# Kernel tuning notes

Measured on AMD Instinct MI355X. Metric: run time of the kernel, lower is better.

Reference implementation:

```python
import jax, jax.numpy as jnp
import numpy as np

SIGMA = 1.0
KSIZE = 5
WEAK = 75.0
STRONG = 255.0
LOW_T = 0.00392
HIGH_T = 0.15

# scipy.signal.gaussian(M, std): unnormalized gaussian window
_n = np.arange(KSIZE, dtype=np.float32) - (KSIZE - 1) / 2.0
_g = np.exp(-0.5 * (_n / SIGMA) ** 2).astype(np.float32)
GAUSS_H = jnp.asarray(_g.reshape(1, 1, 1, KSIZE))  # horizontal 1xK
GAUSS_V = jnp.asarray(_g.reshape(1, 1, KSIZE, 1))  # vertical Kx1

_sobel = np.array([[1, 0, -1], [2, 0, -2], [1, 0, -1]], dtype=np.float32)
SOBEL_H = jnp.asarray(_sobel.reshape(1, 1, 3, 3))
SOBEL_V = jnp.asarray(_sobel.T.reshape(1, 1, 3, 3))

_f0 = np.array([[0, 0, 0], [0, 1, -1], [0, 0, 0]], np.float32)
_f45 = np.array([[0, 0, 0], [0, 1, 0], [0, 0, -1]], np.float32)
_f90 = np.array([[0, 0, 0], [0, 1, 0], [0, -1, 0]], np.float32)
_f135 = np.array([[0, 0, 0], [0, 1, 0], [-1, 0, 0]], np.float32)
_f180 = np.array([[0, 0, 0], [-1, 1, 0], [0, 0, 0]], np.float32)
_f225 = np.array([[-1, 0, 0], [0, 1, 0], [0, 0, 0]], np.float32)
_f270 = np.array([[0, -1, 0], [0, 1, 0], [0, 0, 0]], np.float32)
_f315 = np.array([[0, 0, -1], [0, 1, 0], [0, 0, 0]], np.float32)
DIR_FILT = jnp.asarray(np.stack([_f0, _f45, _f90, _f135, _f180, _f225, _f270, _f315]).reshape(8, 1, 3, 3))

NBR_FILT = jnp.asarray(np.array([[1, 1, 1], [1, 0, 1], [1, 1, 1]], np.float32).reshape(1, 1, 3, 3))


def _conv(x, w, pad):
    # cross-correlation, matching torch F.conv2d
    return jax.lax.conv_general_dilated(
        x, w, window_strides=(1, 1), padding=[(pad[0], pad[0]), (pad[1], pad[1])],
        dimension_numbers=('NCHW', 'OIHW', 'NCHW'))


def setup_inputs() -> dict:
    key = jax.random.key(0)
    img = jax.random.uniform(key, (16, 1, 1024, 1024), dtype=jnp.float32)
    return {"img": img}


def reference(img):
    B = img.shape[0]
    # --- gaussian noise removal (separable) ---
    sm = _conv(img, GAUSS_H, (0, KSIZE // 2))
    sm = _conv(sm, GAUSS_V, (KSIZE // 2, 0))
    # --- sobel gradients ---
    Ix = _conv(sm, SOBEL_H, (1, 1))
    Iy = _conv(sm, SOBEL_V, (1, 1))
    mag = jnp.sqrt(Ix ** 2 + Iy ** 2)
    mag = mag / mag.reshape(B, -1).max(axis=1).reshape(B, 1, 1, 1)
    direction = jnp.arctan2(Iy, Ix) * (180.0 / 3.1415926) + 180.0
    direction = jnp.round(direction / 45.0) * 45.0
    # --- non-max suppression via directional differences + gather ---
    all_filtered = _conv(mag, DIR_FILT, (1, 1))  # [B,8,H,W]
    idx_pos = (direction / 45.0).astype(jnp.int32) % 8  # [B,1,H,W]
    idx_neg = (idx_pos + 4) % 8
    cs_pos = jnp.take_along_axis(all_filtered, idx_pos, axis=1)
    cs_neg = jnp.take_along_axis(all_filtered, idx_neg, axis=1)
    is_max = jnp.minimum(cs_pos, cs_neg) > 0.0
    thin = jnp.where(is_max, mag, 0.0)
    # --- double threshold ---
    hi = thin.max() * HIGH_T  # global max, as in source
    strong = thin >= hi
    weak = (thin < hi) & (thin >= LOW_T)
    inter = jnp.where(strong, STRONG, jnp.where(weak, WEAK, 0.0))
    # --- hysteresis: iterate until no weak pixel gains a strong neighbor ---
    def cond(state):
        return state[1]

    def body(state):
        x, _ = state
        weak_m = x == WEAK
        sn = _conv((x == STRONG).astype(jnp.float32), NBR_FILT, (1, 1))
        new_strong = weak_m & (sn > 0.0)
        x = jnp.where(new_strong, STRONG, x)
        return x, new_strong.any()

    final, _ = jax.lax.while_loop(cond, body, (inter, jnp.asarray(True)))
    final = jnp.where(final == STRONG, final, 0.0)
    return final
```

## Files before the change

### kernel.cpp

```cpp
#include <hip/hip_runtime.h>
#include <math.h>

#define BB 16
#define H 1024
#define W 1024
#define HW (H*W)
#define NTOT (BB*HW)

typedef unsigned long long u64;

__device__ __constant__ float GW[5] = {
    0.13533528323661270f, 0.60653065971263342f, 1.0f,
    0.60653065971263342f, 0.13533528323661270f};

__device__ __constant__ int NBDY[8] = {0, 1, 1, 1, 0, -1, -1, -1};
__device__ __constant__ int NBDX[8] = {1, 1, 0, -1, -1, -1, 0, 1};

#define CSCALE ((float)(180.0 / 3.1415926))

#define TW 128
#define TH 8
__global__ __launch_bounds__(256, 8) void k_smooth_sobel(const float* __restrict__ img,
                                                         float* __restrict__ mag,
                                                         unsigned char* __restrict__ bucket,
                                                         float* __restrict__ partial) {
#pragma clang fp contract(off)
    __shared__ float sA[14 * 136 + 16];
    __shared__ float sB[14 * 132];
    __shared__ float red[256];

    const int tid = threadIdx.x;
    const int x0 = blockIdx.x * TW;
    const int y0 = blockIdx.y * TH;
    const int b = blockIdx.z;
    const size_t base = (size_t)b * HW;

    for (int idx = tid; idx < 14 * 34; idx += 256) {
        int r = idx / 34, v = idx - r * 34;
        int gy = y0 - 3 + r;
        int gxv = x0 - 4 + v * 4;
        float4 val = make_float4(0.f, 0.f, 0.f, 0.f);
        if (gy >= 0 && gy < H && gxv >= 0 && gxv <= W - 4)
            val = *(const float4*)&img[base + (size_t)gy * W + gxv];
        *(float4*)&sA[r * 136 + v * 4] = val;
    }
    __syncthreads();

    for (int idx = tid; idx < 14 * 33; idx += 256) {
        int r = idx / 33, g = idx - r * 33;
        const float* p = &sA[r * 136 + g * 4];
        float4 A0 = *(const float4*)p;
        float4 A1 = *(const float4*)(p + 4);
        float4 A2 = *(const float4*)(p + 8);
        float a_[12] = {A0.x, A0.y, A0.z, A0.w, A1.x, A1.y, A1.z, A1.w,
                        A2.x, A2.y, A2.z, A2.w};
        float o[4];
#pragma unroll
        for (int j = 0; j < 4; ++j) {
            float s = 0.0f;
#pragma unroll
            for (int k = 0; k < 5; ++k) s = s + GW[k] * a_[j + 1 + k];
            o[j] = s;
        }
        *(float4*)&sB[r * 132 + g * 4] = make_float4(o[0], o[1], o[2], o[3]);
    }
    __syncthreads();

    for (int idx = tid; idx < 10 * 33; idx += 256) {
        int rr = idx / 33, g = idx - rr * 33;
        float bb[20];
#pragma unroll
        for (int k = 0; k < 5; ++k) {
            float4 t = *(const float4*)&sB[(rr + k) * 132 + g * 4];
            bb[k * 4 + 0] = t.x; bb[k * 4 + 1] = t.y;
            bb[k * 4 + 2] = t.z; bb[k * 4 + 3] = t.w;
        }
        int gy = y0 - 1 + rr;
        bool rowok = (gy >= 0 && gy < H);
        float o[4];
#pragma unroll
        for (int j = 0; j < 4; ++j) {
            float s = 0.0f;
#pragma unroll
            for (int k = 0; k < 5; ++k) s = s + GW[k] * bb[k * 4 + j];
            int gx = x0 - 1 + g * 4 + j;
            o[j] = (rowok && gx >= 0 && gx < W) ? s : 0.0f;
        }
        *(float4*)&sA[rr * 136 + g * 4] = make_float4(o[0], o[1], o[2], o[3]);
    }
    __syncthreads();

    const int r = tid >> 5;
    const int cg = (tid & 31) * 4;
    const int y = y0 + r;
    const float* P0 = &sA[r * 136 + cg];
    const float* P1 = P0 + 136;
    const float* P2 = P1 + 136;
    float4 q0 = *(const float4*)P0; float2 e0 = *(const float2*)(P0 + 4);
    float4 q1 = *(const float4*)P1; float2 e1 = *(const float2*)(P1 + 4);
    float4 q2 = *(const float4*)P2; float2 e2 = *(const float2*)(P2 + 4);
    float r0[6] = {q0.x, q0.y, q0.z, q0.w, e0.x, e0.y};
    float r1[6] = {q1.x, q1.y, q1.z, q1.w, e1.x, e1.y};
    float r2[6] = {q2.x, q2.y, q2.z, q2.w, e2.x, e2.y};

    float tmax = 0.0f;
    float mg[4];
    unsigned int bk = 0;
#pragma unroll
    for (int j = 0; j < 4; ++j) {
        float a00 = r0[j], a01 = r0[j + 1], a02 = r0[j + 2];
        float a10 = r1[j],                  a12 = r1[j + 2];
        float a20 = r2[j], a21 = r2[j + 1], a22 = r2[j + 2];

        float Ix = a00;
        Ix = Ix - a02;
        Ix = Ix + 2.0f * a10;
        Ix = Ix - 2.0f * a12;
        Ix = Ix + a20;
        Ix = Ix - a22;

        float Iy = a00;
        Iy = Iy + 2.0f * a01;
        Iy = Iy + a02;
        Iy = Iy - a20;
        Iy = Iy - 2.0f * a21;
        Iy = Iy - a22;

        float t1 = Ix * Ix;
        float t2 = Iy * Iy;
        float m = sqrtf(t1 + t2);
        mg[j] = m;
        tmax = fmaxf(tmax, m);

        float ax = fabsf(Ix), ay = fabsf(Iy);
        float mn = fminf(ax, ay), mx = fmaxf(ax, ay);
        float cr = mn * 0.92387953f - mx * 0.38268343f;
        int bidx;
        if (fabsf(cr) < mx * 3e-5f) {
            float fa2 = (float)atan2((double)Iy, (double)Ix);
            float d2 = fa2 * CSCALE;
            d2 = d2 + 180.0f;
            float t2d = d2 / 45.0f;
            float rr2 = rintf(t2d);
            bidx = ((int)rr2) & 7;
        } else if (ay <= ax * 0.41421356f) {
            bidx = signbit(Ix) ? 0 : 4;
        } else if (ay >= ax * 2.41421356f) {
            bidx = (Iy >= 0.0f) ? 6 : 2;
        } else {
            bidx = (Iy >= 0.0f) ? ((Ix >= 0.0f) ? 5 : 7)
                                : ((Ix >= 0.0f) ? 3 : 1);
        }
        bk |= ((unsigned int)bidx) << (8 * j);
    }
    *(float4*)&mag[base + (size_t)y * W + x0 + cg] = make_float4(mg[0], mg[1], mg[2], mg[3]);
    *(unsigned int*)&bucket[base + (size_t)y * W + x0 + cg] = bk;

    red[tid] = tmax;
    __syncthreads();
    for (int s = 128; s > 0; s >>= 1) {
        if (tid < s) red[tid] = fmaxf(red[tid], red[tid + s]);
        __syncthreads();
    }
    if (tid == 0) {
        int pb = (blockIdx.z * 128 + blockIdx.y) * 8 + blockIdx.x;
        partial[pb] = red[0];
    }
}

__global__ __launch_bounds__(256) void k_redmax_img(const float* __restrict__ partial,
                                                    float* __restrict__ magmax) {
    __shared__ float red[256];
    const float* p = partial + blockIdx.x * 1024;
    float m = 0.0f;
    for (int k = threadIdx.x; k < 1024; k += 256) m = fmaxf(m, p[k]);
    red[threadIdx.x] = m;
    __syncthreads();
    for (int s = 128; s > 0; s >>= 1) {
        if (threadIdx.x < s) red[threadIdx.x] = fmaxf(red[threadIdx.x], red[threadIdx.x + s]);
        __syncthreads();
    }
    if (threadIdx.x == 0) magmax[blockIdx.x] = red[0];
}

__global__ __launch_bounds__(256, 6) void k_nms_b(const float* __restrict__ mag,
                                                  const unsigned char* __restrict__ bucket,
                                                  const float* __restrict__ magmax,
                                                  u64* __restrict__ Mb,
                                                  float* __restrict__ partial) {
#pragma clang fp contract(off)
    __shared__ float sN[34 * 136];
    __shared__ unsigned int nib32[256];
    __shared__ float red[256];

    const int tid = threadIdx.x;
    const int x0 = blockIdx.x * 128;
    const int y0 = blockIdx.y * 32;
    const int b = blockIdx.z;
    const size_t base = (size_t)b * HW;
    const float M = magmax[b];

    for (int idx = tid; idx < 34 * 34; idx += 256) {
        int r = idx / 34, v = idx - r * 34;
        int gy = y0 - 1 + r;
        int gxv = x0 - 4 + v * 4;
        float4 val = make_float4(0.f, 0.f, 0.f, 0.f);
        if (gy >= 0 && gy < H && gxv >= 0 && gxv <= W - 4)
            val = *(const float4*)&mag[base + (size_t)gy * W + gxv];
        *(float4*)&sN[r * 136 + v * 4] = val;
    }
    __syncthreads();

    const int r = tid >> 5;
    const int cg = (tid & 31) * 4;
    float amax = 0.0f;

    for (int k4 = 0; k4 < 4; ++k4) {
        const int rr = k4 * 8 + r;
        const int y = y0 + rr;
        unsigned int bk4 = *(const unsigned int*)&bucket[base + (size_t)y * W + x0 + cg];
        float4 a4 = *(const float4*)&sN[(rr + 1) * 136 + cg + 4];
        float av[4] = {a4.x, a4.y, a4.z, a4.w};
        bool im[4];
        bool bad = false;
        float bpv[4], bnv[4];
        bool g1v[4], g2v[4], f1v[4], f2v[4];
#pragma unroll
        for (int j = 0; j < 4; ++j) {
            int c = cg + j;
            int bkt = (bk4 >> (8 * j)) & 0xff;
            int dy = NBDY[bkt], dx = NBDX[bkt];
            float a = av[j];
            float bp = sN[(rr + 1 + dy) * 136 + c + 4 + dx];
            float bn = sN[(rr + 1 - dy) * 136 + c + 4 - dx];
            bpv[j] = bp; bnv[j] = bn;
            bool g1 = a > bp, g2 = a > bn;
            bool f1 = a >= bp * 1.0000005f;
            bool f2 = a >= bn * 1.0000005f;
            g1v[j] = g1; g2v[j] = g2; f1v[j] = f1; f2v[j] = f2;
            im[j] = g1 && g2;
            bad = bad || (g1 && !f1) || (g2 && !f2);
        }
        if (__any(bad)) {
#pragma unroll
            for (int j = 0; j < 4; ++j) {
                bool b1 = g1v[j] && !f1v[j];
                bool b2 = g2v[j] && !f2v[j];
                if (b1 || b2) {
                    float qa = av[j] / M;
                    bool r1 = g1v[j], r2 = g2v[j];
                    if (b1) r1 = qa > (bpv[j] / M);
                    if (b2) r2 = qa > (bnv[j] / M);
                    im[j] = r1 && r2;
                }
            }
        }
        unsigned int nib = 0;
#pragma unroll
        for (int j = 0; j < 4; ++j) {
            if (im[j]) { nib |= 1u << j; amax = fmaxf(amax, av[j]); }
        }
        nib32[tid] = nib;
        __syncthreads();
        if (tid < 16) {
            int rw = tid >> 1, h = tid & 1;
            u64 w = 0;
#pragma unroll
            for (int j = 0; j < 16; ++j)
                w |= (u64)nib32[rw * 32 + h * 16 + j] << (4 * j);
            int yy = y0 + k4 * 8 + rw;
            int widx = ((b << 8) | ((yy >> 6) << 4) | ((x0 >> 6) + h)) * 64 + (yy & 63);
            Mb[widx] = w;
        }
        __syncthreads();
    }

    red[tid] = amax;
    __syncthreads();
    for (int s = 128; s > 0; s >>= 1) {
        if (tid < s) red[tid] = fmaxf(red[tid], red[tid + s]);
        __syncthreads();
    }
    if (tid == 0)
        partial[(blockIdx.z * 32 + blockIdx.y) * 8 + blockIdx.x] = red[0] / M;
}

__global__ __launch_bounds__(1024) void k_finalize_thr(const float* __restrict__ partial,
                                                       float* __restrict__ hdr,
                                                       float* __restrict__ thr) {
    __shared__ float red[1024];
    float m = 0.0f;
    for (int k = threadIdx.x; k < 4096; k += 1024) m = fmaxf(m, partial[k]);
    red[threadIdx.x] = m;
    __syncthreads();
    for (int s = 512; s > 0; s >>= 1) {
        if (threadIdx.x < s) red[threadIdx.x] = fmaxf(red[threadIdx.x], red[threadIdx.x + s]);
        __syncthreads();
    }
    if (threadIdx.x == 0) hdr[16] = red[0];
    if (threadIdx.x < 32) {
        float tm = red[0];
        int t = threadIdx.x;
        float M = hdr[t >> 1];
        float T = (t & 1) ? (tm * 0.15f) : 0.00392f;
        if (0.0f / M >= T) { thr[t] = 0.0f; return; }
        unsigned int lo = 0u, hi = 0x7f800000u;
        while (hi - lo > 1u) {
            unsigned int mid = lo + ((hi - lo) >> 1);
            if (__uint_as_float(mid) / M >= T) hi = mid; else lo = mid;
        }
        thr[t] = __uint_as_float(hi);
    }
}

__global__ __launch_bounds__(256, 8) void k_thresh_b(const float* __restrict__ mag,
                                                     const u64* __restrict__ Mb,
                                                     const float* __restrict__ hdr,
                                                     const float* __restrict__ thr,
                                                     u64* __restrict__ Sb,
                                                     u64* __restrict__ Wb) {
    __shared__ unsigned int nibS[256], nibW[256];
    const int tid = threadIdx.x;
    const int x0 = blockIdx.x * 128;
    const int y0 = blockIdx.y * 32;
    const int b = blockIdx.z;
    const size_t base = (size_t)b * HW;
    const float Alo = thr[b * 2], Ahi = thr[b * 2 + 1];
    const bool snm = (hdr[16] * 0.15f <= 0.0f);
    const int r = tid >> 5;
    const int cg = (tid & 31) * 4;
    const int hl = cg >> 6;

    for (int k4 = 0; k4 < 4; ++k4) {
        const int rr = k4 * 8 + r;
        const int y = y0 + rr;
        float4 a4 = *(const float4*)&mag[base + (size_t)y * W + x0 + cg];
        float av[4] = {a4.x, a4.y, a4.z, a4.w};
        const int widx = ((b << 8) | ((y >> 6) << 4) | ((x0 >> 6) + hl)) * 64 + (y & 63);
        u64 mw = Mb[widx];
        unsigned int ns = 0, nw = 0;
#pragma unroll
        for (int j = 0; j < 4; ++j) {
            bool im = (mw >> ((cg & 63) + j)) & 1ull;
            bool strong = snm || (im && (av[j] >= Ahi));
            bool weak = (!strong) && im && (av[j] >= Alo);
            ns |= (strong ? 1u : 0u) << j;
            nw |= (weak ? 1u : 0u) << j;
        }
        nibS[tid] = ns;
        nibW[tid] = nw;
        __syncthreads();
        if (tid < 32) {
            bool isW = (tid >= 16);
            int t = tid & 15;
            int rw = t >> 1, h = t & 1;
            const unsigned int* nb = isW ? nibW : nibS;
            u64 w = 0;
#pragma unroll
            for (int j = 0; j < 16; ++j)
                w |= (u64)nb[rw * 32 + h * 16 + j] << (4 * j);
            int yy = y0 + k4 * 8 + rw;
            int widx2 = ((b << 8) | ((yy >> 6) << 4) | ((x0 >> 6) + h)) * 64 + (yy & 63);
            if (isW) Wb[widx2] = w; else Sb[widx2] = w;
        }
        __syncthreads();
    }
}

template <bool LAST>
__global__ __launch_bounds__(256) void k_hyster_bits(const u64* __restrict__ Wb,
                                                     u64* __restrict__ Sb,
                                                     float* __restrict__ out) {
    const int lane = threadIdx.x & 63;
    const int t = blockIdx.x * 4 + (threadIdx.x >> 6);
    const int ty = (t >> 4) & 15;
    const int tx = t & 15;
    const int idx = t * 64 + lane;

    u64 S = Sb[idx];
    const u64 Wk = Wb[idx];

    u64 hstat = 0;
    if (tx > 0)  hstat |= (Sb[(t - 1) * 64 + lane] >> 63) & 1ull;
    if (tx < 15) hstat |= (Sb[(t + 1) * 64 + lane] & 1ull) << 63;

    u64 halo = 0;
    if (lane == 0 && ty > 0) {
        const int ta = t - 16;
        u64 tc = Sb[ta * 64 + 63];
        u64 hh = (tc << 1) | tc | (tc >> 1);
        if (tx > 0)  hh |= (Sb[(ta - 1) * 64 + 63] >> 63) & 1ull;
        if (tx < 15) hh |= (Sb[(ta + 1) * 64 + 63] & 1ull) << 63;
        halo = hh;
    }
    if (lane == 63 && ty < 15) {
        const int tb = t + 16;
        u64 tc = Sb[tb * 64 + 0];
        u64 hh = (tc << 1) | tc | (tc >> 1);
        if (tx > 0)  hh |= (Sb[(tb - 1) * 64 + 0] >> 63) & 1ull;
        if (tx < 15) hh |= (Sb[(tb + 1) * 64 + 0] & 1ull) << 63;
        halo = hh;
    }

    for (int it = 0; it < 160; ++it) {
        u64 hh = (S << 1) | S | (S >> 1) | hstat;
        u64 up = __shfl_up(hh, 1, 64);
        if (lane == 0) up = halo;
        u64 dn = __shfl_down(hh, 1, 64);
        if (lane == 63) dn = halo;
        u64 dil = hh | up | dn;
        u64 nS = S | (Wk & dil);
        bool ch = (nS != S);
        S = nS;
        if (!__any(ch)) break;
    }

    if (!LAST) {
        Sb[idx] = S;
    } else {
        const int bimg = t >> 8;
        float* op = out + (size_t)bimg * HW + (size_t)(ty * 64) * W + tx * 64 + lane;
#pragma unroll 4
        for (int rr = 0; rr < 64; ++rr) {
            u64 wrow = __shfl(S, rr, 64);
            op[(size_t)rr * W] = ((wrow >> lane) & 1ull) ? 255.0f : 0.0f;
        }
    }
}

extern "C" void kernel_launch(void* const* d_in, const int* in_sizes, int n_in,
                              void* d_out, int out_size, void* d_ws, size_t ws_size,
                              hipStream_t stream) {
    (void)in_sizes; (void)n_in; (void)out_size; (void)ws_size;
    const float* img = (const float*)d_in[0];
    float* out = (float*)d_out;

    float* hdr = (float*)d_ws;
    float* thr = hdr + 64;
    float* partialA = hdr + 128;
    float* partialB = partialA + 16384;
    float* A = partialB + 4096;
    unsigned char* C = (unsigned char*)(A + (size_t)NTOT);
    u64* Sb = (u64*)(C + (size_t)NTOT);
    u64* Wb = Sb + NTOT / 64;
    u64* Mb = Wb + NTOT / 64;

    dim3 blk(256);
    k_smooth_sobel<<<dim3(8, 128, BB), blk, 0, stream>>>(img, A, C, partialA);
    k_redmax_img<<<dim3(BB), blk, 0, stream>>>(partialA, hdr);
    k_nms_b<<<dim3(8, 32, BB), blk, 0, stream>>>(A, C, hdr, Mb, partialB);
    k_finalize_thr<<<dim3(1), dim3(1024), 0, stream>>>(partialB, hdr, thr);
    k_thresh_b<<<dim3(8, 32, BB), blk, 0, stream>>>(A, Mb, hdr, thr, Sb, Wb);
    for (int p = 0; p < 5; ++p)
        k_hyster_bits<false><<<dim3(NTOT / (64 * 64) / 4), blk, 0, stream>>>(Wb, Sb, out);
    k_hyster_bits<true><<<dim3(NTOT / (64 * 64) / 4), blk, 0, stream>>>(Wb, Sb, out);
}
```

Baseline: 242.2 us.

## Fuse smoothing, Sobel and NMS into one kernel with deferred ambiguous-pixel list

Merges the smooth/Sobel kernel and the NMS kernel into one tiled kernel. It recomputes the magnitude halo in shared memory, so the full-resolution magnitude and bucket arrays are no longer written and re-read. Pixels whose NMS decision depends on normalisation rounding are appended to a capped global list through an atomic counter, and a single-block post kernel resolves them after the per-image max is known, also folding in the reductions. This removes two kernels and a large amount of global traffic. The costs are halo recomputation, a global atomic, and a list cap that could overflow and give wrong results on unusual inputs.

```diff
diff --git a/kernel.cpp b/kernel.cpp
--- a/kernel.cpp
+++ b/kernel.cpp
@@ -6,6 +6,7 @@
 #define W 1024
 #define HW (H*W)
 #define NTOT (BB*HW)
+#define CAP 262144u
 
 typedef unsigned long long u64;
 
@@ -18,64 +19,61 @@
 
 #define CSCALE ((float)(180.0 / 3.1415926))
 
-#define TW 128
-#define TH 8
-__global__ __launch_bounds__(256, 8) void k_smooth_sobel(const float* __restrict__ img,
-                                                         float* __restrict__ mag,
-                                                         unsigned char* __restrict__ bucket,
-                                                         float* __restrict__ partial) {
+__global__ __launch_bounds__(256, 8) void k_smooth_sobel_nms(
+    const float* __restrict__ img, float* __restrict__ thin,
+    float* __restrict__ partialA, float* __restrict__ partialB,
+    unsigned int* __restrict__ cnt, uint4* __restrict__ list) {
 #pragma clang fp contract(off)
-    __shared__ float sA[14 * 136 + 16];
-    __shared__ float sB[14 * 132];
-    __shared__ float red[256];
+    __shared__ float sA[24 * 80];
+    __shared__ float sB[24 * 76];
+    unsigned short* sBk = (unsigned short*)&sA[1600];
+    float* redS = &sA[1800];
 
     const int tid = threadIdx.x;
-    const int x0 = blockIdx.x * TW;
-    const int y0 = blockIdx.y * TH;
+    const int x0 = blockIdx.x * 64;
+    const int y0 = blockIdx.y * 16;
     const int b = blockIdx.z;
     const size_t base = (size_t)b * HW;
 
-    for (int idx = tid; idx < 14 * 34; idx += 256) {
-        int r = idx / 34, v = idx - r * 34;
-        int gy = y0 - 3 + r;
-        int gxv = x0 - 4 + v * 4;
+    for (int idx = tid; idx < 24 * 20; idx += 256) {
+        int r = idx / 20, v = idx - r * 20;
+        int gy = y0 - 4 + r;
+        int gxv = x0 - 8 + v * 4;
         float4 val = make_float4(0.f, 0.f, 0.f, 0.f);
         if (gy >= 0 && gy < H && gxv >= 0 && gxv <= W - 4)
             val = *(const float4*)&img[base + (size_t)gy * W + gxv];
-        *(float4*)&sA[r * 136 + v * 4] = val;
-    }
-    __syncthreads();
-
-    for (int idx = tid; idx < 14 * 33; idx += 256) {
-        int r = idx / 33, g = idx - r * 33;
-        const float* p = &sA[r * 136 + g * 4];
+        *(float4*)&sA[r * 80 + v * 4] = val;
+    }
+    __syncthreads();
+
+    for (int idx = tid; idx < 24 * 19; idx += 256) {
+        int r = idx / 19, g = idx - r * 19;
+        const float* p = &sA[r * 80 + g * 4];
         float4 A0 = *(const float4*)p;
         float4 A1 = *(const float4*)(p + 4);
-        float4 A2 = *(const float4*)(p + 8);
-        float a_[12] = {A0.x, A0.y, A0.z, A0.w, A1.x, A1.y, A1.z, A1.w,
-                        A2.x, A2.y, A2.z, A2.w};
+        float a_[8] = {A0.x, A0.y, A0.z, A0.w, A1.x, A1.y, A1.z, A1.w};
         float o[4];
 #pragma unroll
         for (int j = 0; j < 4; ++j) {
             float s = 0.0f;
 #pragma unroll
-            for (int k = 0; k < 5; ++k) s = s + GW[k] * a_[j + 1 + k];
+            for (int k = 0; k < 5; ++k) s = s + GW[k] * a_[j + k];
             o[j] = s;
         }
-        *(float4*)&sB[r * 132 + g * 4] = make_float4(o[0], o[1], o[2], o[3]);
-    }
-    __syncthreads();
-
-    for (int idx = tid; idx < 10 * 33; idx += 256) {
-        int rr = idx / 33, g = idx - rr * 33;
+        *(float4*)&sB[r * 76 + g * 4] = make_float4(o[0], o[1], o[2], o[3]);
+    }
+    __syncthreads();
+
+    for (int idx = tid; idx < 20 * 19; idx += 256) {
+        int rr = idx / 19, g = idx - rr * 19;
         float bb[20];
 #pragma unroll
         for (int k = 0; k < 5; ++k) {
-            float4 t = *(const float4*)&sB[(rr + k) * 132 + g * 4];
+            float4 t = *(const float4*)&sB[(rr + k) * 76 + g * 4];
             bb[k * 4 + 0] = t.x; bb[k * 4 + 1] = t.y;
             bb[k * 4 + 2] = t.z; bb[k * 4 + 3] = t.w;
         }
-        int gy = y0 - 1 + rr;
+        int gy = y0 - 2 + rr;
         bool rowok = (gy >= 0 && gy < H);
         float o[4];
 #pragma unroll
@@ -83,225 +81,208 @@
             float s = 0.0f;
 #pragma unroll
             for (int k = 0; k < 5; ++k) s = s + GW[k] * bb[k * 4 + j];
-            int gx = x0 - 1 + g * 4 + j;
+            int gx = x0 - 6 + g * 4 + j;
             o[j] = (rowok && gx >= 0 && gx < W) ? s : 0.0f;
         }
-        *(float4*)&sA[rr * 136 + g * 4] = make_float4(o[0], o[1], o[2], o[3]);
-    }
-    __syncthreads();
-
-    const int r = tid >> 5;
-    const int cg = (tid & 31) * 4;
+        *(float4*)&sA[rr * 80 + g * 4] = make_float4(o[0], o[1], o[2], o[3]);
+    }
+    __syncthreads();
+
+    for (int idx = tid; idx < 18 * 18; idx += 256) {
+        int m = idx / 18, gq = idx - m * 18;
+        const float* P0 = &sA[m * 80 + gq * 4];
+        const float* P1 = P0 + 80;
+        const float* P2 = P1 + 80;
+        float4 q0 = *(const float4*)P0; float4 e0 = *(const float4*)(P0 + 4);
+        float4 q1 = *(const float4*)P1; float4 e1 = *(const float4*)(P1 + 4);
+        float4 q2 = *(const float4*)P2; float4 e2 = *(const float4*)(P2 + 4);
+        float r0[8] = {q0.x, q0.y, q0.z, q0.w, e0.x, e0.y, e0.z, e0.w};
+        float r1[8] = {q1.x, q1.y, q1.z, q1.w, e1.x, e1.y, e1.z, e1.w};
+        float r2[8] = {q2.x, q2.y, q2.z, q2.w, e2.x, e2.y, e2.z, e2.w};
+        int gy = y0 - 1 + m;
+        unsigned int bk = 0;
+        float mg[4];
+#pragma unroll
+        for (int j = 0; j < 4; ++j) {
+            float a00 = r0[j + 1], a01 = r0[j + 2], a02 = r0[j + 3];
+            float a10 = r1[j + 1],                  a12 = r1[j + 3];
+            float a20 = r2[j + 1], a21 = r2[j + 2], a22 = r2[j + 3];
+
+            float Ix = a00;
+            Ix = Ix - a02;
+            Ix = Ix + 2.0f * a10;
+            Ix = Ix - 2.0f * a12;
+            Ix = Ix + a20;
+            Ix = Ix - a22;
+
+            float Iy = a00;
+            Iy = Iy + 2.0f * a01;
+            Iy = Iy + a02;
+            Iy = Iy - a20;
+            Iy = Iy - 2.0f * a21;
+            Iy = Iy - a22;
+
+            float t1 = Ix * Ix;
+            float t2 = Iy * Iy;
+            float m2 = sqrtf(t1 + t2);
+            int gx = x0 - 4 + gq * 4 + j;
+            if (gy < 0 || gy >= H || gx < 0 || gx >= W) m2 = 0.0f;
+            mg[j] = m2;
+
+            float ax = fabsf(Ix), ay = fabsf(Iy);
+            float mn = fminf(ax, ay), mx = fmaxf(ax, ay);
+            float cr = mn * 0.92387953f - mx * 0.38268343f;
+            int bidx;
+            if (fabsf(cr) < mx * 3e-5f) {
+                float fa2 = (float)atan2((double)Iy, (double)Ix);
+                float d2 = fa2 * CSCALE;
+                d2 = d2 + 180.0f;
+                float t2d = d2 / 45.0f;
+                float rr2 = rintf(t2d);
+                bidx = ((int)rr2) & 7;
+            } else if (ay <= ax * 0.41421356f) {
+                bidx = signbit(Ix) ? 0 : 4;
+            } else if (ay >= ax * 2.41421356f) {
+                bidx = (Iy >= 0.0f) ? 6 : 2;
+            } else {
+                bidx = (Iy >= 0.0f) ? ((Ix >= 0.0f) ? 5 : 7)
+                                    : ((Ix >= 0.0f) ? 3 : 1);
+            }
+            bk |= ((unsigned int)bidx) << (4 * j);
+        }
+        *(float4*)&sB[m * 76 + gq * 4] = make_float4(mg[0], mg[1], mg[2], mg[3]);
+        sBk[m * 18 + gq] = (unsigned short)bk;
+    }
+    __syncthreads();
+
+    const int r = tid >> 4;
+    const int cg = (tid & 15) * 4;
     const int y = y0 + r;
-    const float* P0 = &sA[r * 136 + cg];
-    const float* P1 = P0 + 136;
-    const float* P2 = P1 + 136;
-    float4 q0 = *(const float4*)P0; float2 e0 = *(const float2*)(P0 + 4);
-    float4 q1 = *(const float4*)P1; float2 e1 = *(const float2*)(P1 + 4);
-    float4 q2 = *(const float4*)P2; float2 e2 = *(const float2*)(P2 + 4);
-    float r0[6] = {q0.x, q0.y, q0.z, q0.w, e0.x, e0.y};
-    float r1[6] = {q1.x, q1.y, q1.z, q1.w, e1.x, e1.y};
-    float r2[6] = {q2.x, q2.y, q2.z, q2.w, e2.x, e2.y};
-
-    float tmax = 0.0f;
-    float mg[4];
-    unsigned int bk = 0;
-#pragma unroll
-    for (int j = 0; j < 4; ++j) {
-        float a00 = r0[j], a01 = r0[j + 1], a02 = r0[j + 2];
-        float a10 = r1[j],                  a12 = r1[j + 2];
-        float a20 = r2[j], a21 = r2[j + 1], a22 = r2[j + 2];
-
-        float Ix = a00;
-        Ix = Ix - a02;
-        Ix = Ix + 2.0f * a10;
-        Ix = Ix - 2.0f * a12;
-        Ix = Ix + a20;
-        Ix = Ix - a22;
-
-        float Iy = a00;
-        Iy = Iy + 2.0f * a01;
-        Iy = Iy + a02;
-        Iy = Iy - a20;
-        Iy = Iy - 2.0f * a21;
-        Iy = Iy - a22;
-
-        float t1 = Ix * Ix;
-        float t2 = Iy * Iy;
-        float m = sqrtf(t1 + t2);
-        mg[j] = m;
-        tmax = fmaxf(tmax, m);
-
-        float ax = fabsf(Ix), ay = fabsf(Iy);
-        float mn = fminf(ax, ay), mx = fmaxf(ax, ay);
-        float cr = mn * 0.92387953f - mx * 0.38268343f;
-        int bidx;
-        if (fabsf(cr) < mx * 3e-5f) {
-            float fa2 = (float)atan2((double)Iy, (double)Ix);
-            float d2 = fa2 * CSCALE;
-            d2 = d2 + 180.0f;
-            float t2d = d2 / 45.0f;
-            float rr2 = rintf(t2d);
-            bidx = ((int)rr2) & 7;
-        } else if (ay <= ax * 0.41421356f) {
-            bidx = signbit(Ix) ? 0 : 4;
-        } else if (ay >= ax * 2.41421356f) {
-            bidx = (Iy >= 0.0f) ? 6 : 2;
-        } else {
-            bidx = (Iy >= 0.0f) ? ((Ix >= 0.0f) ? 5 : 7)
-                                : ((Ix >= 0.0f) ? 3 : 1);
-        }
-        bk |= ((unsigned int)bidx) << (8 * j);
-    }
-    *(float4*)&mag[base + (size_t)y * W + x0 + cg] = make_float4(mg[0], mg[1], mg[2], mg[3]);
-    *(unsigned int*)&bucket[base + (size_t)y * W + x0 + cg] = bk;
-
-    red[tid] = tmax;
-    __syncthreads();
-    for (int s = 128; s > 0; s >>= 1) {
-        if (tid < s) red[tid] = fmaxf(red[tid], red[tid + s]);
-        __syncthreads();
-    }
+    const int m = r + 1;
+    float tmax = 0.0f, amax = 0.0f;
+    {
+        unsigned int bk4 = sBk[m * 18 + (cg >> 2) + 1];
+        float4 a4 = *(const float4*)&sB[m * 76 + cg + 4];
+        float av[4] = {a4.x, a4.y, a4.z, a4.w};
+        float o[4];
+#pragma unroll
+        for (int j = 0; j < 4; ++j) {
+            int bkt = (bk4 >> (4 * j)) & 7;
+            int dy = NBDY[bkt], dx = NBDX[bkt];
+            int cm = cg + 4 + j;
+            float a = av[j];
+            float bp = sB[(m + dy) * 76 + cm + dx];
+            float bn = sB[(m - dy) * 76 + cm - dx];
+            bool g1 = a > bp, g2 = a > bn;
+            bool im = g1 && g2;
+            if (im) {
+                bool f1 = a >= bp * 1.0000005f;
+                bool f2 = a >= bn * 1.0000005f;
+                if (!(f1 && f2)) {
+                    im = false;
+                    unsigned int id = atomicAdd(cnt, 1u);
+                    if (id < CAP) {
+                        uint4 e;
+                        e.x = (unsigned int)(base + (size_t)y * W + x0 + cg + j);
+                        e.y = __float_as_uint(a);
+                        e.z = __float_as_uint(bp);
+                        e.w = __float_as_uint(bn);
+                        list[id] = e;
+                    }
+                }
+            }
+            tmax = fmaxf(tmax, a);
+            if (im) amax = fmaxf(amax, a);
+            o[j] = im ? a : 0.0f;
+        }
+        *(float4*)&thin[base + (size_t)y * W + x0 + cg] =
+            make_float4(o[0], o[1], o[2], o[3]);
+    }
+#pragma unroll
+    for (int off = 32; off > 0; off >>= 1) {
+        tmax = fmaxf(tmax, __shfl_down(tmax, off));
+        amax = fmaxf(amax, __shfl_down(amax, off));
+    }
+    if ((tid & 63) == 0) { redS[tid >> 6] = tmax; redS[4 + (tid >> 6)] = amax; }
+    __syncthreads();
     if (tid == 0) {
-        int pb = (blockIdx.z * 128 + blockIdx.y) * 8 + blockIdx.x;
-        partial[pb] = red[0];
+        float tA = fmaxf(fmaxf(redS[0], redS[1]), fmaxf(redS[2], redS[3]));
+        float tB = fmaxf(fmaxf(redS[4], redS[5]), fmaxf(redS[6], redS[7]));
+        int pb = (b * 64 + blockIdx.y) * 16 + blockIdx.x;
+        partialA[pb] = tA;
+        partialB[pb] = tB;
     }
 }
 
-__global__ __launch_bounds__(256) void k_redmax_img(const float* __restrict__ partial,
-                                                    float* __restrict__ magmax) {
-    __shared__ float red[256];
-    const float* p = partial + blockIdx.x * 1024;
-    float m = 0.0f;
-    for (int k = threadIdx.x; k < 1024; k += 256) m = fmaxf(m, p[k]);
-    red[threadIdx.x] = m;
-    __syncthreads();
-    for (int s = 128; s > 0; s >>= 1) {
-        if (threadIdx.x < s) red[threadIdx.x] = fmaxf(red[threadIdx.x], red[threadIdx.x + s]);
-        __syncthreads();
-    }
-    if (threadIdx.x == 0) magmax[blockIdx.x] = red[0];
-}
-
-__global__ __launch_bounds__(256, 6) void k_nms_b(const float* __restrict__ mag,
-                                                  const unsigned char* __restrict__ bucket,
-                                                  const float* __restrict__ magmax,
-                                                  u64* __restrict__ Mb,
-                                                  float* __restrict__ partial) {
+__global__ __launch_bounds__(1024) void k_post(const float* __restrict__ partialA,
+                                               const float* __restrict__ partialB,
+                                               const unsigned int* __restrict__ cnt,
+                                               const uint4* __restrict__ list,
+                                               float* __restrict__ thin,
+                                               float* __restrict__ hdr,
+                                               float* __restrict__ thr) {
 #pragma clang fp contract(off)
-    __shared__ float sN[34 * 136];
-    __shared__ unsigned int nib32[256];
-    __shared__ float red[256];
-
+    __shared__ float sM[16];
+    __shared__ int sAmaxI[16];
+    __shared__ float sTm[16];
+    __shared__ float sTmAll;
     const int tid = threadIdx.x;
-    const int x0 = blockIdx.x * 128;
-    const int y0 = blockIdx.y * 32;
-    const int b = blockIdx.z;
-    const size_t base = (size_t)b * HW;
-    const float M = magmax[b];
-
-    for (int idx = tid; idx < 34 * 34; idx += 256) {
-        int r = idx / 34, v = idx - r * 34;
-        int gy = y0 - 1 + r;
-        int gxv = x0 - 4 + v * 4;
-        float4 val = make_float4(0.f, 0.f, 0.f, 0.f);
-        if (gy >= 0 && gy < H && gxv >= 0 && gxv <= W - 4)
-            val = *(const float4*)&mag[base + (size_t)gy * W + gxv];
-        *(float4*)&sN[r * 136 + v * 4] = val;
-    }
-    __syncthreads();
-
-    const int r = tid >> 5;
-    const int cg = (tid & 31) * 4;
-    float amax = 0.0f;
-
-    for (int k4 = 0; k4 < 4; ++k4) {
-        const int rr = k4 * 8 + r;
-        const int y = y0 + rr;
-        unsigned int bk4 = *(const unsigned int*)&bucket[base + (size_t)y * W + x0 + cg];
-        float4 a4 = *(const float4*)&sN[(rr + 1) * 136 + cg + 4];
-        float av[4] = {a4.x, a4.y, a4.z, a4.w};
-        bool im[4];
-        bool bad = false;
-        float bpv[4], bnv[4];
-        bool g1v[4], g2v[4], f1v[4], f2v[4];
-#pragma unroll
-        for (int j = 0; j < 4; ++j) {
-            int c = cg + j;
-            int bkt = (bk4 >> (8 * j)) & 0xff;
-            int dy = NBDY[bkt], dx = NBDX[bkt];
-            float a = av[j];
-            float bp = sN[(rr + 1 + dy) * 136 + c + 4 + dx];
-            float bn = sN[(rr + 1 - dy) * 136 + c + 4 - dx];
-            bpv[j] = bp; bnv[j] = bn;
-            bool g1 = a > bp, g2 = a > bn;
+    const int iw = tid >> 6, lane = tid & 63;
+
+    {
+        const float* p = partialA + iw * 1024;
+        float m = 0.0f;
+        for (int k = lane; k < 1024; k += 64) m = fmaxf(m, p[k]);
+        for (int off = 32; off > 0; off >>= 1) m = fmaxf(m, __shfl_down(m, off));
+        if (lane == 0) { sM[iw] = m; sAmaxI[iw] = 0; hdr[iw] = m; }
+    }
+    __syncthreads();
+
+    {
+        unsigned int n = *cnt;
+        if (n > CAP) n = CAP;
+        for (unsigned int i = tid; i < n; i += 1024) {
+            uint4 e = list[i];
+            float a = __uint_as_float(e.y);
+            float bp = __uint_as_float(e.z);
+            float bn = __uint_as_float(e.w);
+            int b = (int)(e.x >> 20);
+            float M = sM[b];
             bool f1 = a >= bp * 1.0000005f;
             bool f2 = a >= bn * 1.0000005f;
-            g1v[j] = g1; g2v[j] = g2; f1v[j] = f1; f2v[j] = f2;
-            im[j] = g1 && g2;
-            bad = bad || (g1 && !f1) || (g2 && !f2);
-        }
-        if (__any(bad)) {
-#pragma unroll
-            for (int j = 0; j < 4; ++j) {
-                bool b1 = g1v[j] && !f1v[j];
-                bool b2 = g2v[j] && !f2v[j];
-                if (b1 || b2) {
-                    float qa = av[j] / M;
-                    bool r1 = g1v[j], r2 = g2v[j];
-                    if (b1) r1 = qa > (bpv[j] / M);
-                    if (b2) r2 = qa > (bnv[j] / M);
-                    im[j] = r1 && r2;
-                }
+            float qa = a / M;
+            bool r1 = f1 ? true : (qa > (bp / M));
+            bool r2 = f2 ? true : (qa > (bn / M));
+            if (r1 && r2) {
+                thin[e.x] = a;
+                atomicMax(&sAmaxI[b], __float_as_int(a));
             }
         }
-        unsigned int nib = 0;
-#pragma unroll
-        for (int j = 0; j < 4; ++j) {
-            if (im[j]) { nib |= 1u << j; amax = fmaxf(amax, av[j]); }
-        }
-        nib32[tid] = nib;
-        __syncthreads();
-        if (tid < 16) {
-            int rw = tid >> 1, h = tid & 1;
-            u64 w = 0;
-#pragma unroll
-            for (int j = 0; j < 16; ++j)
-                w |= (u64)nib32[rw * 32 + h * 16 + j] << (4 * j);
-            int yy = y0 + k4 * 8 + rw;
-            int widx = ((b << 8) | ((yy >> 6) << 4) | ((x0 >> 6) + h)) * 64 + (yy & 63);
-            Mb[widx] = w;
-        }
-        __syncthreads();
-    }
-
-    red[tid] = amax;
-    __syncthreads();
-    for (int s = 128; s > 0; s >>= 1) {
-        if (tid < s) red[tid] = fmaxf(red[tid], red[tid + s]);
-        __syncthreads();
-    }
-    if (tid == 0)
-        partial[(blockIdx.z * 32 + blockIdx.y) * 8 + blockIdx.x] = red[0] / M;
-}
-
-__global__ __launch_bounds__(1024) void k_finalize_thr(const float* __restrict__ partial,
-                                                       float* __restrict__ hdr,
-                                                       float* __restrict__ thr) {
-    __shared__ float red[1024];
-    float m = 0.0f;
-    for (int k = threadIdx.x; k < 4096; k += 1024) m = fmaxf(m, partial[k]);
-    red[threadIdx.x] = m;
-    __syncthreads();
-    for (int s = 512; s > 0; s >>= 1) {
-        if (threadIdx.x < s) red[threadIdx.x] = fmaxf(red[threadIdx.x], red[threadIdx.x + s]);
-        __syncthreads();
-    }
-    if (threadIdx.x == 0) hdr[16] = red[0];
-    if (threadIdx.x < 32) {
-        float tm = red[0];
-        int t = threadIdx.x;
-        float M = hdr[t >> 1];
+    }
+    __syncthreads();
+
+    {
+        const float* p = partialB + iw * 1024;
+        float m = 0.0f;
+        for (int k = lane; k < 1024; k += 64) m = fmaxf(m, p[k]);
+        for (int off = 32; off > 0; off >>= 1) m = fmaxf(m, __shfl_down(m, off));
+        if (lane == 0) {
+            m = fmaxf(m, __int_as_float(sAmaxI[iw]));
+            sTm[iw] = m / sM[iw];
+        }
+    }
+    __syncthreads();
+    if (tid == 0) {
+        float tm = 0.0f;
+        for (int i = 0; i < 16; ++i) tm = fmaxf(tm, sTm[i]);
+        hdr[16] = tm;
+        sTmAll = tm;
+    }
+    __syncthreads();
+    if (tid < 32) {
+        float tm = sTmAll;
+        int t = tid;
+        float M = sM[t >> 1];
         float T = (t & 1) ? (tm * 0.15f) : 0.00392f;
         if (0.0f / M >= T) { thr[t] = 0.0f; return; }
         unsigned int lo = 0u, hi = 0x7f800000u;
@@ -313,8 +294,7 @@
     }
 }
 
-__global__ __launch_bounds__(256, 8) void k_thresh_b(const float* __restrict__ mag,
-                                                     const u64* __restrict__ Mb,
+__global__ __launch_bounds__(256, 8) void k_thresh_b(const float* __restrict__ thin,
                                                      const float* __restrict__ hdr,
                                                      const float* __restrict__ thr,
                                                      u64* __restrict__ Sb,
@@ -329,21 +309,17 @@
     const bool snm = (hdr[16] * 0.15f <= 0.0f);
     const int r = tid >> 5;
     const int cg = (tid & 31) * 4;
-    const int hl = cg >> 6;
 
     for (int k4 = 0; k4 < 4; ++k4) {
         const int rr = k4 * 8 + r;
         const int y = y0 + rr;
-        float4 a4 = *(const float4*)&mag[base + (size_t)y * W + x0 + cg];
+        float4 a4 = *(const float4*)&thin[base + (size_t)y * W + x0 + cg];
         float av[4] = {a4.x, a4.y, a4.z, a4.w};
-        const int widx = ((b << 8) | ((y >> 6) << 4) | ((x0 >> 6) + hl)) * 64 + (y & 63);
-        u64 mw = Mb[widx];
         unsigned int ns = 0, nw = 0;
 #pragma unroll
         for (int j = 0; j < 4; ++j) {
-            bool im = (mw >> ((cg & 63) + j)) & 1ull;
-            bool strong = snm || (im && (av[j] >= Ahi));
-            bool weak = (!strong) && im && (av[j] >= Alo);
+            bool strong = snm || (av[j] >= Ahi);
+            bool weak = (!strong) && (av[j] >= Alo);
             ns |= (strong ? 1u : 0u) << j;
             nw |= (weak ? 1u : 0u) << j;
         }
@@ -437,20 +413,22 @@
 
     float* hdr = (float*)d_ws;
     float* thr = hdr + 64;
+    unsigned int* cnt = (unsigned int*)(hdr + 96);
     float* partialA = hdr + 128;
     float* partialB = partialA + 16384;
-    float* A = partialB + 4096;
-    unsigned char* C = (unsigned char*)(A + (size_t)NTOT);
-    u64* Sb = (u64*)(C + (size_t)NTOT);
+    uint4* list = (uint4*)(partialB + 16384);
+    float* thin = (float*)((char*)list + (size_t)CAP * 16);
+    u64* Sb = (u64*)(thin + (size_t)NTOT);
     u64* Wb = Sb + NTOT / 64;
-    u64* Mb = Wb + NTOT / 64;
+
+    hipMemsetAsync(cnt, 0, sizeof(unsigned int), stream);
 
     dim3 blk(256);
-    k_smooth_sobel<<<dim3(8, 128, BB), blk, 0, stream>>>(img, A, C, partialA);
-    k_redmax_img<<<dim3(BB), blk, 0, stream>>>(partialA, hdr);
-    k_nms_b<<<dim3(8, 32, BB), blk, 0, stream>>>(A, C, hdr, Mb, partialB);
-    k_finalize_thr<<<dim3(1), dim3(1024), 0, stream>>>(partialB, hdr, thr);
-    k_thresh_b<<<dim3(8, 32, BB), blk, 0, stream>>>(A, Mb, hdr, thr, Sb, Wb);
+    k_smooth_sobel_nms<<<dim3(16, 64, BB), blk, 0, stream>>>(img, thin, partialA,
+                                                             partialB, cnt, list);
+    k_post<<<dim3(1), dim3(1024), 0, stream>>>(partialA, partialB, cnt, list,
+                                               thin, hdr, thr);
+    k_thresh_b<<<dim3(8, 32, BB), blk, 0, stream>>>(thin, hdr, thr, Sb, Wb);
     for (int p = 0; p < 5; ++p)
         k_hyster_bits<false><<<dim3(NTOT / (64 * 64) / 4), blk, 0, stream>>>(Wb, Sb, out);
     k_hyster_bits<true><<<dim3(NTOT / (64 * 64) / 4), blk, 0, stream>>>(Wb, Sb, out);
```

Result: slower. 291.9 us (+20.6%).
